# Optimization experiments

Measured on AMD Instinct MI355X. Metric: run time of the kernel, lower is better.

The kernel has to match this reference:

```python
import jax, jax.numpy as jnp
import numpy as np

# CustomConvLayer with a 3x3-tap .kof file, global defaults:
#   operation: x * w, input_encode: x, kernel_encode: w
# => out[b,o,h,w] = sum_c sum_k x_pad[b,c,h+dh_k,w+dw_k] * weights[o,c,k]
# Tap offsets: integer stencil (dh,dw) in {0,1,2}^2 (k_elems=9), padding=1, stride=1.

PAD = 1
TAPS = [(dh, dw) for dh in range(3) for dw in range(3)]  # 9 taps


def setup_inputs() -> dict:
    key = jax.random.key(0)
    k1, k2 = jax.random.split(key)
    x = jax.random.normal(k1, (16, 64, 128, 128), dtype=jnp.float32)
    # learned per-tap weights: [out_channels, in_channels, k_elems]
    weights = jax.random.normal(k2, (128, 64, 9), dtype=jnp.float32) * 0.05
    return {"x": x, "weights": weights}


def reference(x, weights):
    B, C, H, Wd = x.shape
    xp = jnp.pad(x, ((0, 0), (0, 0), (PAD, PAD), (PAD, PAD)))
    # gather per-tap shifted views: [B, C, K, H, W]
    gathered = jnp.stack([xp[:, :, dh:dh + H, dw:dw + Wd] for dh, dw in TAPS], axis=2)
    # per-tap op x*w, then combine over in_channels and taps
    out = jnp.einsum('bckhw,ock->bohw', gathered, weights)
    return out
```

## Files before the change

kernel.cpp:

```cpp
#include <hip/hip_runtime.h>
#include <hip/hip_bf16.h>
#include <stdint.h>


typedef __bf16 bf16x8 __attribute__((ext_vector_type(8)));
typedef float  f32x4  __attribute__((ext_vector_type(4)));

__global__ __launch_bounds__(256) void xform_w(const float* __restrict__ wgt,
                                               __bf16* __restrict__ BtF) {
  const int t = blockIdx.x * 256 + threadIdx.x;
  if (t >= 9216) return;
  const int s = t >> 9, rem = t & 511, quad = rem >> 7, n = rem & 127;
  bf16x8 o;
#pragma unroll
  for (int r = 0; r < 8; ++r) {
    const int k = s * 32 + quad * 8 + r;
    const int tap = k >> 6, c = k & 63;
    o[r] = (__bf16)wgt[(n * 64 + c) * 9 + tap];
  }
  *(bf16x8*)(BtF + (size_t)t * 8) = o;
}

__global__ __launch_bounds__(256) void conv_mfma(const float* __restrict__ x,
                                                 const __bf16* __restrict__ BtF,
                                                 float* __restrict__ out) {
  __shared__ alignas(16) __bf16 Aslab[3120 * 8];
  const int tid  = threadIdx.x;
  const int lane = tid & 63;
  const int wave = tid >> 6;
  const int quad = lane >> 4;
  const int l16  = lane & 15;
  const int rank = (blockIdx.x & 7) * 256 + (blockIdx.x >> 3);
  const int b = rank >> 7;
  const int h = rank & 127;
  const int wm = wave >> 1;
  const int wn = wave & 1;

  if (tid < 48) {
    const int r3 = tid >> 4, wp = ((tid >> 3) & 1) * 129, cq = tid & 7;
    const int v = r3 * 130 + wp;
    const bf16x8 z = {};
    *(bf16x8*)(Aslab + (size_t)(v * 8 + (cq ^ (v & 7))) * 8) = z;
  }

  const int c8 = tid >> 5;
  const int wl = tid & 31;
  const float* xb = x + ((size_t)b * 64 + c8 * 8) * 16384 + wl;

  float f[4][8];

#define T_ISSUE(T) do {                                                       \
    const int u_ = (T) >> 2, p_ = (T) & 3;                                    \
    const int xr_ = h - 1 + u_;                                               \
    if (xr_ >= 0 && xr_ <= 127) {                                             \
      const float* p0_ = xb + (size_t)xr_ * 128 + p_ * 32;                    \
      _Pragma("unroll")                                                       \
      for (int cc = 0; cc < 8; ++cc) f[(T) & 3][cc] = p0_[(size_t)cc * 16384];\
    }                                                                         \
  } while (0)

#define T_CONSUME(T) do {                                                     \
    const int u_ = (T) >> 2, p_ = (T) & 3;                                    \
    const int xr_ = h - 1 + u_;                                               \
    bf16x8 pk = {};                                                           \
    if (xr_ >= 0 && xr_ <= 127) {                                             \
      _Pragma("unroll")                                                       \
      for (int cc = 0; cc < 8; ++cc) pk[cc] = (__bf16)f[(T) & 3][cc];         \
    }                                                                         \
    const int v_ = u_ * 130 + 1 + p_ * 32 + wl;                               \
    *(bf16x8*)(Aslab + (size_t)(v_ * 8 + (c8 ^ (v_ & 7))) * 8) = pk;          \
  } while (0)

  T_ISSUE(0); T_ISSUE(1); T_ISSUE(2);
#pragma unroll
  for (int t = 0; t < 12; ++t) {
    if (t < 9) T_ISSUE(t + 3);
    T_CONSUME(t);
  }
  __syncthreads();

  f32x4 acc[4][4] = {};
#pragma unroll
  for (int s = 0; s < 18; ++s) {
    const int tap = s >> 1;
    const int dh = tap / 3, dw = tap % 3;
    const int cq = ((s & 1) << 2) + quad;
    bf16x8 aF[4], bF[4];
#pragma unroll
    for (int i = 0; i < 4; ++i) {
      const int m = (wm << 6) + (i << 4) + l16;
      const int v = dh * 130 + m + dw;
      const int slot = (v << 3) + (cq ^ (v & 7));
      aF[i] = *(const bf16x8*)(Aslab + (size_t)slot * 8);
      const int n = (wn << 6) + (i << 4) + l16;
      bF[i] = *(const bf16x8*)(BtF + ((size_t)((s * 4 + quad) * 128 + n) << 3));
    }
#pragma unroll
    for (int i = 0; i < 4; ++i)
#pragma unroll
      for (int j = 0; j < 4; ++j)
        acc[i][j] = __builtin_amdgcn_mfma_f32_16x16x32_bf16(aF[i], bF[j], acc[i][j], 0, 0, 0);
  }

#pragma unroll
  for (int j = 0; j < 4; ++j) {
    const int n = (wn << 6) + (j << 4) + l16;
    float* orow = out + (((size_t)(b * 128 + n) * 128 + h) << 7);
#pragma unroll
    for (int i = 0; i < 4; ++i) {
      const int m0 = (wm << 6) + (i << 4) + (quad << 2);
      *(f32x4*)(orow + m0) = acc[i][j];
    }
  }
}

__global__ void conv_naive(const float* __restrict__ x, const float* __restrict__ wgt,
                           float* __restrict__ out, int total) {
  int idx = blockIdx.x * 256 + threadIdx.x;
  if (idx >= total) return;
  const int w = idx & 127;
  const int h = (idx >> 7) & 127;
  const int o = (idx >> 14) & 127;
  const int b = idx >> 21;
  float s = 0.f;
  for (int c = 0; c < 64; ++c) {
    const float* xc = x + ((size_t)(b * 64 + c) * 128) * 128;
    const float* wc = wgt + (o * 64 + c) * 9;
    for (int dh = 0; dh < 3; ++dh) {
      const int hh = h + dh - 1;
      if (hh < 0 || hh >= 128) continue;
      for (int dw = 0; dw < 3; ++dw) {
        const int ww = w + dw - 1;
        if (ww < 0 || ww >= 128) continue;
        s += xc[hh * 128 + ww] * wc[dh * 3 + dw];
      }
    }
  }
  out[idx] = s;
}

extern "C" void kernel_launch(void* const* d_in, const int* in_sizes, int n_in,
                              void* d_out, int out_size, void* d_ws, size_t ws_size,
                              hipStream_t stream) {
  const float* x   = (const float*)d_in[0];
  const float* wgt = (const float*)d_in[1];
  float* out = (float*)d_out;

  const size_t BTF_BYTES = 9216ull * 16;

  if (ws_size < BTF_BYTES) {
    const int total = 16 * 128 * 128 * 128;
    conv_naive<<<(total + 255) / 256, 256, 0, stream>>>(x, wgt, out, total);
    return;
  }

  __bf16* BtF = (__bf16*)d_ws;

  xform_w<<<36, 256, 0, stream>>>(wgt, BtF);
  conv_mfma<<<2048, 256, 0, stream>>>(x, BtF, out);
}
```

Measured before the change: 219.6 us.

## Issue all input loads up front and prefetch weight fragments three steps ahead

All twelve global input row loads are now issued before any conversion. Before, only three were in flight at a time, so this exposes more memory-level parallelism. Weight fragments are register-prefetched three K-steps ahead of the MFMA loop, and the first three prefetches are issued before the barrier. Launch bounds now request 3 blocks per SM. This raises register pressure (96 floats plus 16 bf16x8 buffers), which could cause spills or limit occupancy.

```diff
diff --git a/kernel.cpp b/kernel.cpp
--- a/kernel.cpp
+++ b/kernel.cpp
@@ -21,9 +21,9 @@
   *(bf16x8*)(BtF + (size_t)t * 8) = o;
 }
 
-__global__ __launch_bounds__(256) void conv_mfma(const float* __restrict__ x,
-                                                 const __bf16* __restrict__ BtF,
-                                                 float* __restrict__ out) {
+__global__ __launch_bounds__(256, 3) void conv_mfma(const float* __restrict__ x,
+                                                    const __bf16* __restrict__ BtF,
+                                                    float* __restrict__ out) {
   __shared__ alignas(16) __bf16 Aslab[3120 * 8];
   const int tid  = threadIdx.x;
   const int lane = tid & 63;
@@ -47,7 +47,7 @@
   const int wl = tid & 31;
   const float* xb = x + ((size_t)b * 64 + c8 * 8) * 16384 + wl;
 
-  float f[4][8];
+  float f[12][8];
 
 #define T_ISSUE(T) do {                                                       \
     const int u_ = (T) >> 2, p_ = (T) & 3;                                    \
@@ -55,7 +55,7 @@
     if (xr_ >= 0 && xr_ <= 127) {                                             \
       const float* p0_ = xb + (size_t)xr_ * 128 + p_ * 32;                    \
       _Pragma("unroll")                                                       \
-      for (int cc = 0; cc < 8; ++cc) f[(T) & 3][cc] = p0_[(size_t)cc * 16384];\
+      for (int cc = 0; cc < 8; ++cc) f[(T)][cc] = p0_[(size_t)cc * 16384];    \
     }                                                                         \
   } while (0)
 
@@ -65,41 +65,53 @@
     bf16x8 pk = {};                                                           \
     if (xr_ >= 0 && xr_ <= 127) {                                             \
       _Pragma("unroll")                                                       \
-      for (int cc = 0; cc < 8; ++cc) pk[cc] = (__bf16)f[(T) & 3][cc];         \
+      for (int cc = 0; cc < 8; ++cc) pk[cc] = (__bf16)f[(T)][cc];             \
     }                                                                         \
     const int v_ = u_ * 130 + 1 + p_ * 32 + wl;                               \
     *(bf16x8*)(Aslab + (size_t)(v_ * 8 + (c8 ^ (v_ & 7))) * 8) = pk;          \
   } while (0)
 
-  T_ISSUE(0); T_ISSUE(1); T_ISSUE(2);
 #pragma unroll
-  for (int t = 0; t < 12; ++t) {
-    if (t < 9) T_ISSUE(t + 3);
-    T_CONSUME(t);
-  }
+  for (int t = 0; t < 12; ++t) T_ISSUE(t);
+#pragma unroll
+  for (int t = 0; t < 12; ++t) T_CONSUME(t);
+
+  bf16x8 bR[4][4];
+#define BLOAD(S) do {                                                         \
+    if ((S) < 18) {                                                           \
+      _Pragma("unroll")                                                       \
+      for (int i = 0; i < 4; ++i) {                                           \
+        const int n_ = (wn << 6) + (i << 4) + l16;                            \
+        bR[(S) & 3][i] = *(const bf16x8*)(BtF +                               \
+            ((size_t)(((S) * 4 + quad) * 128 + n_) << 3));                    \
+      }                                                                       \
+    }                                                                         \
+  } while (0)
+
+  BLOAD(0); BLOAD(1); BLOAD(2);
   __syncthreads();
 
   f32x4 acc[4][4] = {};
 #pragma unroll
   for (int s = 0; s < 18; ++s) {
+    BLOAD(s + 3);
     const int tap = s >> 1;
     const int dh = tap / 3, dw = tap % 3;
     const int cq = ((s & 1) << 2) + quad;
-    bf16x8 aF[4], bF[4];
+    bf16x8 aF[4];
 #pragma unroll
     for (int i = 0; i < 4; ++i) {
       const int m = (wm << 6) + (i << 4) + l16;
       const int v = dh * 130 + m + dw;
       const int slot = (v << 3) + (cq ^ (v & 7));
       aF[i] = *(const bf16x8*)(Aslab + (size_t)slot * 8);
-      const int n = (wn << 6) + (i << 4) + l16;
-      bF[i] = *(const bf16x8*)(BtF + ((size_t)((s * 4 + quad) * 128 + n) << 3));
     }
 #pragma unroll
     for (int i = 0; i < 4; ++i)
 #pragma unroll
       for (int j = 0; j < 4; ++j)
-        acc[i][j] = __builtin_amdgcn_mfma_f32_16x16x32_bf16(aF[i], bF[j], acc[i][j], 0, 0, 0);
+        acc[i][j] = __builtin_amdgcn_mfma_f32_16x16x32_bf16(aF[i], bR[s & 3][j],
+                                                            acc[i][j], 0, 0, 0);
   }
 
 #pragma unroll
```

Result: no change. 221.5 us (+0.9%).

## Use 512-thread blocks with 8 waves splitting output tile and staging loads

Applied to the files above, without the earlier changes.

Doubles the conv block to 8 waves, so each wave computes a 32x64 output sub-tile instead of 64x64. This halves per-wave accumulators and MFMA work. The staging of the input row slab is reorganised so each wave loads one 8-channel group across 64 columns in 6 steps, replacing the software-pipelined issue/consume macro scheme. The aim is more waves in flight to hide latency and lower register pressure, at the cost of duplicated B-fragment loads per wave and losing the explicit load prefetch overlap.

```diff
diff --git a/kernel.cpp b/kernel.cpp
--- a/kernel.cpp
+++ b/kernel.cpp
@@ -21,7 +21,7 @@
   *(bf16x8*)(BtF + (size_t)t * 8) = o;
 }
 
-__global__ __launch_bounds__(256) void conv_mfma(const float* __restrict__ x,
+__global__ __launch_bounds__(512) void conv_mfma(const float* __restrict__ x,
                                                  const __bf16* __restrict__ BtF,
                                                  float* __restrict__ out) {
   __shared__ alignas(16) __bf16 Aslab[3120 * 8];
@@ -33,8 +33,8 @@
   const int rank = (blockIdx.x & 7) * 256 + (blockIdx.x >> 3);
   const int b = rank >> 7;
   const int h = rank & 127;
+  const int wn = wave & 1;
   const int wm = wave >> 1;
-  const int wn = wave & 1;
 
   if (tid < 48) {
     const int r3 = tid >> 4, wp = ((tid >> 3) & 1) * 129, cq = tid & 7;
@@ -43,60 +43,50 @@
     *(bf16x8*)(Aslab + (size_t)(v * 8 + (cq ^ (v & 7))) * 8) = z;
   }
 
-  const int c8 = tid >> 5;
-  const int wl = tid & 31;
+  const int c8 = wave;
+  const int wl = tid & 63;
   const float* xb = x + ((size_t)b * 64 + c8 * 8) * 16384 + wl;
 
-  float f[4][8];
-
-#define T_ISSUE(T) do {                                                       \
-    const int u_ = (T) >> 2, p_ = (T) & 3;                                    \
-    const int xr_ = h - 1 + u_;                                               \
-    if (xr_ >= 0 && xr_ <= 127) {                                             \
-      const float* p0_ = xb + (size_t)xr_ * 128 + p_ * 32;                    \
-      _Pragma("unroll")                                                       \
-      for (int cc = 0; cc < 8; ++cc) f[(T) & 3][cc] = p0_[(size_t)cc * 16384];\
-    }                                                                         \
-  } while (0)
-
-#define T_CONSUME(T) do {                                                     \
-    const int u_ = (T) >> 2, p_ = (T) & 3;                                    \
-    const int xr_ = h - 1 + u_;                                               \
-    bf16x8 pk = {};                                                           \
-    if (xr_ >= 0 && xr_ <= 127) {                                             \
-      _Pragma("unroll")                                                       \
-      for (int cc = 0; cc < 8; ++cc) pk[cc] = (__bf16)f[(T) & 3][cc];         \
-    }                                                                         \
-    const int v_ = u_ * 130 + 1 + p_ * 32 + wl;                               \
-    *(bf16x8*)(Aslab + (size_t)(v_ * 8 + (c8 ^ (v_ & 7))) * 8) = pk;          \
-  } while (0)
-
-  T_ISSUE(0); T_ISSUE(1); T_ISSUE(2);
 #pragma unroll
-  for (int t = 0; t < 12; ++t) {
-    if (t < 9) T_ISSUE(t + 3);
-    T_CONSUME(t);
+  for (int t = 0; t < 6; ++t) {
+    const int r  = t >> 1;
+    const int wh = t & 1;
+    const int xr = h - 1 + r;
+    bf16x8 pk = {};
+    if (xr >= 0 && xr <= 127) {
+      const float* p0 = xb + (size_t)xr * 128 + wh * 64;
+      float f[8];
+#pragma unroll
+      for (int cc = 0; cc < 8; ++cc) f[cc] = p0[(size_t)cc * 16384];
+#pragma unroll
+      for (int cc = 0; cc < 8; ++cc) pk[cc] = (__bf16)f[cc];
+    }
+    const int v = r * 130 + 1 + wh * 64 + wl;
+    *(bf16x8*)(Aslab + (size_t)(v * 8 + (c8 ^ (v & 7))) * 8) = pk;
   }
   __syncthreads();
 
-  f32x4 acc[4][4] = {};
+  f32x4 acc[2][4] = {};
 #pragma unroll
   for (int s = 0; s < 18; ++s) {
     const int tap = s >> 1;
     const int dh = tap / 3, dw = tap % 3;
     const int cq = ((s & 1) << 2) + quad;
-    bf16x8 aF[4], bF[4];
+    bf16x8 aF[2], bF[4];
 #pragma unroll
-    for (int i = 0; i < 4; ++i) {
-      const int m = (wm << 6) + (i << 4) + l16;
+    for (int i = 0; i < 2; ++i) {
+      const int m = (wm << 5) + (i << 4) + l16;
       const int v = dh * 130 + m + dw;
       const int slot = (v << 3) + (cq ^ (v & 7));
       aF[i] = *(const bf16x8*)(Aslab + (size_t)slot * 8);
-      const int n = (wn << 6) + (i << 4) + l16;
-      bF[i] = *(const bf16x8*)(BtF + ((size_t)((s * 4 + quad) * 128 + n) << 3));
     }
 #pragma unroll
-    for (int i = 0; i < 4; ++i)
+    for (int j = 0; j < 4; ++j) {
+      const int n = (wn << 6) + (j << 4) + l16;
+      bF[j] = *(const bf16x8*)(BtF + ((size_t)((s * 4 + quad) * 128 + n) << 3));
+    }
+#pragma unroll
+    for (int i = 0; i < 2; ++i)
 #pragma unroll
       for (int j = 0; j < 4; ++j)
         acc[i][j] = __builtin_amdgcn_mfma_f32_16x16x32_bf16(aF[i], bF[j], acc[i][j], 0, 0, 0);
@@ -107,8 +97,8 @@
     const int n = (wn << 6) + (j << 4) + l16;
     float* orow = out + (((size_t)(b * 128 + n) * 128 + h) << 7);
 #pragma unroll
-    for (int i = 0; i < 4; ++i) {
-      const int m0 = (wm << 6) + (i << 4) + (quad << 2);
+    for (int i = 0; i < 2; ++i) {
+      const int m0 = (wm << 5) + (i << 4) + (quad << 2);
       *(f32x4*)(orow + m0) = acc[i][j];
     }
   }
@@ -157,5 +147,5 @@
   __bf16* BtF = (__bf16*)d_ws;
 
   xform_w<<<36, 256, 0, stream>>>(wgt, BtF);
-  conv_mfma<<<2048, 256, 0, stream>>>(x, BtF, out);
+  conv_mfma<<<2048, 512, 0, stream>>>(x, BtF, out);
 }
```

Result: slower. 234.0 us (+6.6%).

## Stage weight fragments into LDS via async global-to-LDS loads with triple buffering

Applied to the files above, without the earlier changes.

Instead of each wave reading B (weight) fragments straight from global memory every k-step, the kernel now streams each k-step's weight slice into a 3-deep LDS ring using global_load_lds, issued two steps ahead. Manual vmcnt/lgkmcnt waits and a barrier per step replace the single syncthreads. The aim is to hide weight-load latency behind MFMA work and to share each weight slice across waves instead of reloading it per wave. The cost is a larger LDS footprint, which may reduce occupancy, plus a barrier on every step. Correctness depends on the hand-counted vmcnt values.

```diff
diff --git a/kernel.cpp b/kernel.cpp
--- a/kernel.cpp
+++ b/kernel.cpp
@@ -5,6 +5,10 @@
 
 typedef __bf16 bf16x8 __attribute__((ext_vector_type(8)));
 typedef float  f32x4  __attribute__((ext_vector_type(4)));
+
+#define GLD_TO_LDS16(g, l)                                                        \
+  __builtin_amdgcn_global_load_lds((const __attribute__((address_space(1))) void*)(g), \
+                                   (__attribute__((address_space(3))) void*)(l), 16, 0, 0)
 
 __global__ __launch_bounds__(256) void xform_w(const float* __restrict__ wgt,
                                                __bf16* __restrict__ BtF) {
@@ -24,7 +28,7 @@
 __global__ __launch_bounds__(256) void conv_mfma(const float* __restrict__ x,
                                                  const __bf16* __restrict__ BtF,
                                                  float* __restrict__ out) {
-  __shared__ alignas(16) __bf16 Aslab[3120 * 8];
+  __shared__ alignas(16) __bf16 Aslab[4672 * 8];
   const int tid  = threadIdx.x;
   const int lane = tid & 63;
   const int wave = tid >> 6;
@@ -77,30 +81,56 @@
     if (t < 9) T_ISSUE(t + 3);
     T_CONSUME(t);
   }
-  __syncthreads();
+  __builtin_amdgcn_sched_barrier(0);
+
+#define STAGE_S(K, U) do {                                                    \
+    GLD_TO_LDS16(BtF + ((size_t)(((K) << 9) + ((U) << 8) + (wave << 6) + lane) << 3), \
+                 (char*)Aslab + ((3136 + (((K) % 3) << 9) + ((U) << 8) + (wave << 6)) << 4)); \
+  } while (0)
+
+  STAGE_S(0, 0); STAGE_S(0, 1);
+  STAGE_S(1, 0); STAGE_S(1, 1);
+  STAGE_S(2, 0); STAGE_S(2, 1);
+  __builtin_amdgcn_sched_barrier(0);
 
   f32x4 acc[4][4] = {};
-#pragma unroll
-  for (int s = 0; s < 18; ++s) {
-    const int tap = s >> 1;
-    const int dh = tap / 3, dw = tap % 3;
-    const int cq = ((s & 1) << 2) + quad;
-    bf16x8 aF[4], bF[4];
-#pragma unroll
-    for (int i = 0; i < 4; ++i) {
-      const int m = (wm << 6) + (i << 4) + l16;
-      const int v = dh * 130 + m + dw;
-      const int slot = (v << 3) + (cq ^ (v & 7));
-      aF[i] = *(const bf16x8*)(Aslab + (size_t)slot * 8);
-      const int n = (wn << 6) + (i << 4) + l16;
-      bF[i] = *(const bf16x8*)(BtF + ((size_t)((s * 4 + quad) * 128 + n) << 3));
-    }
-#pragma unroll
-    for (int i = 0; i < 4; ++i)
-#pragma unroll
-      for (int j = 0; j < 4; ++j)
-        acc[i][j] = __builtin_amdgcn_mfma_f32_16x16x32_bf16(aF[i], bF[j], acc[i][j], 0, 0, 0);
-  }
+
+#define STEP(S, VM) do {                                                       \
+    asm volatile("s_waitcnt vmcnt(" #VM ")" ::: "memory");                     \
+    asm volatile("s_waitcnt lgkmcnt(0)" ::: "memory");                         \
+    __builtin_amdgcn_s_barrier();                                              \
+    __builtin_amdgcn_sched_barrier(0);                                         \
+    if ((S) >= 1 && (S) <= 15) { STAGE_S((S) + 2, 0); STAGE_S((S) + 2, 1); }   \
+    __builtin_amdgcn_sched_barrier(0);                                         \
+    {                                                                          \
+      const int dh_ = (S) / 6, dw_ = ((S) % 6) >> 1, half_ = (S) & 1;          \
+      const int cq_ = (half_ << 2) + quad;                                     \
+      bf16x8 aF[4], bF[4];          \
+      _Pragma("unroll")                                                        \
+      for (int i = 0; i < 4; ++i) {                                            \
+        const int m_    = (wm << 6) + (i << 4) + l16;                          \
+        const int v_    = dh_ * 130 + m_ + dw_;                                \
+        const int slot_ = (v_ << 3) + (cq_ ^ (v_ & 7));                        \
+        aF[i] = *(const bf16x8*)(Aslab + (size_t)slot_ * 8);                   \
+        bF[i] = *(const bf16x8*)(Aslab +                                       \
+            ((size_t)(3136 + (((S) % 3) << 9) + (quad << 7) + (wn << 6) +      \
+                      (i << 4) + l16) << 3));                                  \
+      }                                                                        \
+      _Pragma("unroll")                                                        \
+      for (int i = 0; i < 4; ++i)                                              \
+        _Pragma("unroll")                                                      \
+        for (int j = 0; j < 4; ++j)                                            \
+          acc[i][j] = __builtin_amdgcn_mfma_f32_16x16x32_bf16(aF[i], bF[j],    \
+                                                              acc[i][j], 0, 0, 0); \
+    }                                                                          \
+  } while (0)
+
+  STEP(0, 4);   STEP(1, 2);   STEP(2, 2);
+  STEP(3, 2);   STEP(4, 2);   STEP(5, 2);
+  STEP(6, 2);   STEP(7, 2);   STEP(8, 2);
+  STEP(9, 2);   STEP(10, 2);  STEP(11, 2);
+  STEP(12, 2);  STEP(13, 2);  STEP(14, 2);
+  STEP(15, 2);  STEP(16, 2);  STEP(17, 0);
 
 #pragma unroll
   for (int j = 0; j < 4; ++j) {
```

Result: no change. 218.1 us (-0.7%).
